# Optimization experiments

Hardware: AMD Instinct MI355X
Metric: run time of the kernel (lower is better)

## Reference

```python
import jax, jax.numpy as jnp
import numpy as np

NBINS = (128, 64, 32)
MIN_BIN_WIDTH = 1e-3
MIN_BIN_HEIGHT = 1e-3


def quadratic_spline(inputs, unnorm_widths, unnorm_heights):
    """Piecewise-quadratic CDF spline (nflows-style). inputs: (N,) in [0,1],
    unnorm_widths: (N, nb), unnorm_heights: (N, nb+1). Returns (outputs, logabsdet)."""
    num_bins = unnorm_widths.shape[-1]
    widths = jax.nn.softmax(unnorm_widths, axis=-1)
    widths = MIN_BIN_WIDTH + (1.0 - MIN_BIN_WIDTH * num_bins) * widths
    hexp = jnp.exp(unnorm_heights)
    # normalize piecewise-linear pdf to integrate to 1
    area = jnp.sum(0.5 * (hexp[:, :-1] + hexp[:, 1:]) * widths, axis=-1, keepdims=True)
    heights = hexp / area
    heights = MIN_BIN_HEIGHT + (1.0 - MIN_BIN_HEIGHT) * heights
    bin_cdf = jnp.cumsum(0.5 * (heights[:, :-1] + heights[:, 1:]) * widths, axis=-1)
    bin_left_cdf = jnp.pad(bin_cdf.at[:, -1].set(1.0), ((0, 0), (1, 0)))
    bin_loc = jnp.cumsum(widths, axis=-1)
    bin_locations = jnp.pad(bin_loc.at[:, -1].set(1.0), ((0, 0), (1, 0)))
    bin_idx = jnp.clip(jnp.sum((inputs[:, None] >= bin_locations).astype(jnp.int32), axis=-1) - 1,
                       0, num_bins - 1)[:, None]
    take = lambda t, i: jnp.take_along_axis(t, i, axis=-1)[:, 0]
    loc = take(bin_locations, bin_idx)
    w = take(widths, bin_idx)
    cdf = take(bin_left_cdf, bin_idx)
    hl = take(heights, bin_idx)
    hr = take(heights, bin_idx + 1)
    alpha = (inputs - loc) / w
    outputs = jnp.clip(0.5 * (hr - hl) * w * alpha * alpha + hl * w * alpha + cdf, 0.0, 1.0)
    logabsdet = jnp.log(alpha * (hr - hl) + hl)
    return outputs, logabsdet


def _forward(coordinates, clustering, delta_height_weight, delta_baseline_weight,
             unnormalized_heights, unnormalized_widths, baseline_bias,
             genes_oi, local_gene_ix, local_cellxgene_ix, localcellxgene_ix):
    n_total_genes = delta_baseline_weight.shape[0]
    # decoder
    dhw = delta_height_weight[genes_oi]                            # (G, L, K)
    mixture_delta = jnp.einsum('cl,glk->cgk', clustering, dhw)     # (C, G, K)
    baseline_delta = clustering @ delta_baseline_weight.T          # (C, n_total)
    baseline = jax.nn.softmax(jnp.log(baseline_bias)[None, :] + baseline_delta, axis=-1)
    baseline_cuts = baseline.reshape(-1)[localcellxgene_ix]        # (N,)
    delta = mixture_delta.reshape(-1, mixture_delta.shape[-1])[local_cellxgene_ix]  # (N, K)
    gene_global = genes_oi[local_gene_ix]                          # (N,)
    # quadratic spline stack log_prob (base = Uniform[0,1])
    x = coordinates
    logabsdet = jnp.zeros_like(coordinates)
    ho = 0
    wo = 0
    for n in NBINS:
        uh = unnormalized_heights[:, ho:ho + n][gene_global] + delta[:, ho:ho + n]
        uw = unnormalized_widths[:, wo:wo + n - 1][gene_global]
        x, lad = quadratic_spline(x, uw, uh)
        logabsdet = logabsdet + lad
        ho += n
        wo += n - 1
    likelihood_position = logabsdet
    likelihood_region = jnp.log(baseline_cuts) + jnp.log(jnp.asarray(n_total_genes, jnp.float32))
    elbo = -(likelihood_position + likelihood_region).sum()
    # KL regularization (scales = exp(log 1.0) = 1)
    half_log_2pi = float(0.5 * np.log(2.0 * np.pi))
    mixture_kl = -0.5 * dhw * dhw - half_log_2pi
    baseline_kl = -0.5 * jnp.square(delta_baseline_weight[genes_oi]) - half_log_2pi
    return elbo - mixture_kl.sum() - baseline_kl.sum()


def setup_inputs() -> dict:
    key = jax.random.key(0)
    ks = jax.random.split(key, 10)
    N, C, G, NT, L = 500_000, 1000, 500, 10_000, 16
    K = sum(NBINS)                # 224 heights / delta components
    W = sum(n - 1 for n in NBINS)  # 221 widths
    coordinates = jax.random.uniform(ks[0], (N,), jnp.float32, 1e-4, 1.0 - 1e-4)
    cluster_id = jax.random.randint(ks[1], (C,), 0, L)
    clustering = jax.nn.one_hot(cluster_id, L, dtype=jnp.float32)
    genes_oi = jnp.sort(jax.random.permutation(ks[2], NT)[:G]).astype(jnp.int32)
    cell_ix = jax.random.randint(ks[3], (N,), 0, C)
    local_gene_ix = jax.random.randint(ks[4], (N,), 0, G).astype(jnp.int32)
    local_cellxgene_ix = (cell_ix * G + local_gene_ix).astype(jnp.int32)
    localcellxgene_ix = (cell_ix * NT + genes_oi[local_gene_ix]).astype(jnp.int32)
    delta_height_weight = jax.random.normal(ks[5], (NT, L, K), jnp.float32) * 0.05
    delta_baseline_weight = jax.random.uniform(ks[6], (NT, L), jnp.float32, -0.25, 0.25)
    unnormalized_heights = jax.random.normal(ks[7], (NT, K), jnp.float32) * 0.1
    unnormalized_widths = jax.random.normal(ks[8], (NT, W), jnp.float32) * 0.1
    baseline_bias = jax.random.uniform(ks[9], (NT,), jnp.float32, 1e-5, 1.0)
    return {
        'coordinates': coordinates, 'clustering': clustering,
        'delta_height_weight': delta_height_weight,
        'delta_baseline_weight': delta_baseline_weight,
        'unnormalized_heights': unnormalized_heights,
        'unnormalized_widths': unnormalized_widths,
        'baseline_bias': baseline_bias,
        'genes_oi': genes_oi, 'local_gene_ix': local_gene_ix,
        'local_cellxgene_ix': local_cellxgene_ix,
        'localcellxgene_ix': localcellxgene_ix,
    }


def reference(coordinates, clustering, delta_height_weight, delta_baseline_weight,
              unnormalized_heights, unnormalized_widths, baseline_bias,
              genes_oi, local_gene_ix, local_cellxgene_ix, localcellxgene_ix):
    return _forward(coordinates, clustering, delta_height_weight, delta_baseline_weight,
                    unnormalized_heights, unnormalized_widths, baseline_bias,
                    genes_oi, local_gene_ix, local_cellxgene_ix, localcellxgene_ix)
```

## Files before the change

### kernel.cpp

```cpp
#include <hip/hip_runtime.h>
#include <math.h>


#define CAP 192
static constexpr float  F_MBW = 1e-3f;
static constexpr float  F_MBH = 1e-3f;
static constexpr double D_HL2PI = 0.918938533204672741780329736406;


__global__ void __launch_bounds__(256)
kA(const float* __restrict__ clustering, int* __restrict__ cid,
   double* __restrict__ dpart, int* __restrict__ cnt, int C, int L, int P) {
  int bid = blockIdx.x, tid = threadIdx.x;
  if (bid < 4) {
    int c = bid * 256 + tid;
    if (c < C) {
      const float* row = clustering + (size_t)c * L;
      int best = 0; float bv = row[0];
      for (int l = 1; l < L; ++l) { float v = row[l]; if (v > bv) { bv = v; best = l; } }
      cid[c] = best;
    }
  } else {
    if (bid == 4 && tid < 128) dpart[tid] = 0.0;
    int i = (bid - 4) * 256 + tid;
    if (i < P) cnt[i] = 0;
  }
}

__global__ void __launch_bounds__(256)
kB(const float* __restrict__ coords, const int* __restrict__ lgi,
   const int* __restrict__ lcg, const int* __restrict__ cid,
   const float* __restrict__ bb, const float* __restrict__ dbw,
   int* __restrict__ cnt, float* __restrict__ xs, double* __restrict__ dpart,
   int N, int G, int L, int NT, int SCAT) {
  int bid = blockIdx.x;
  if (bid < SCAT) {
    int base = bid * 512;
    #pragma unroll
    for (int q = 0; q < 2; ++q) {
      int n = base + q * 256 + threadIdx.x;
      if (n < N) {
        int pair = lgi[n] * L + cid[lcg[n] / G];
        int pos = atomicAdd(&cnt[pair], 1);
        if (pos < CAP) xs[(size_t)pair * CAP + pos] = coords[n];
      }
    }
  } else {
    int g = (bid - SCAT) * 256 + threadIdx.x;
    float s[16];
    #pragma unroll
    for (int l = 0; l < 16; ++l) s[l] = 0.f;
    if (g < NT) {
      float b = bb[g];
      const float4* row = (const float4*)(dbw + (size_t)g * 16);
      #pragma unroll
      for (int q = 0; q < 4; ++q) {
        float4 v = row[q];
        s[4 * q + 0] = b * expf(v.x); s[4 * q + 1] = b * expf(v.y);
        s[4 * q + 2] = b * expf(v.z); s[4 * q + 3] = b * expf(v.w);
      }
    }
    __shared__ float partl[4][16];
    int lane = threadIdx.x & 63, wv = threadIdx.x >> 6;
    #pragma unroll
    for (int l = 0; l < 16; ++l) {
      float v = s[l];
      for (int off = 32; off; off >>= 1) v += __shfl_xor(v, off);
      if (lane == 0) partl[wv][l] = v;
    }
    __syncthreads();
    if (threadIdx.x < 16) {
      float t = partl[0][threadIdx.x] + partl[1][threadIdx.x]
              + partl[2][threadIdx.x] + partl[3][threadIdx.x];
      atomicAdd(&dpart[threadIdx.x * 8], (double)t);
    }
  }
}

static __device__ __forceinline__ void wscan3(float& x, float& y, float& z, int lane) {
  #pragma unroll
  for (int off = 1; off < 64; off <<= 1) {
    float a = __shfl_up(x, off, 64);
    float b = __shfl_up(y, off, 64);
    float c = __shfl_up(z, off, 64);
    if (lane >= off) { x += a; y += b; z += c; }
  }
}

__global__ void __launch_bounds__(64)
k_pair(const float* __restrict__ uh, const float* __restrict__ uw,
       const float* __restrict__ dhw, const int* __restrict__ genes_oi,
       const float* __restrict__ xs, const int* __restrict__ cnt,
       const float* __restrict__ bb, const float* __restrict__ dbw,
       const double* __restrict__ dpart,
       float* __restrict__ partA, float* __restrict__ partB,
       int L, int K, int W, int NT) {
  int p = blockIdx.x;
  int g = p / L;
  int cl = p - g * L;
  int gg = genes_oi[g];
  const float* uhg  = uh + (size_t)gg * K;
  const float* uwg  = uw + (size_t)gg * W;
  const float* drow = dhw + ((size_t)gg * L + cl) * K;
  int t = threadIdx.x;

  __shared__ float s_loc[224];
  __shared__ float s_cdf[224];
  __shared__ float s_hh[224];
  __shared__ int   grd[224];

  const float chh = 1.0f - F_MBH;
  float d2;

  {
    const float cw128 = 1.0f - F_MBW * 127.0f;
    int i0 = 2 * t, i1 = 2 * t + 1;
    float2 dv = *(const float2*)(drow + i0);
    float2 uv = *(const float2*)(uhg + i0);
    d2 = dv.x * dv.x + dv.y * dv.y;
    float h0 = expf(uv.x + dv.x), h1 = expf(uv.y + dv.y);
    float h2 = __shfl_down(h0, 1, 64);
    float ew0 = expf(uwg[i0]);
    float ew1 = (i1 < 127) ? expf(uwg[i1]) : 0.f;
    float a0 = 0.5f * (h0 + h1);
    float a1 = (i1 < 127) ? 0.5f * (h1 + h2) : 0.f;
    float b0 = a0 * ew0, b1 = a1 * ew1;
    float sew = ew0 + ew1, sa = a0 + a1, sb = b0 + b1;
    wscan3(sew, sa, sb, t);
    float wsum = __shfl(sew, 63);
    float S1   = __shfl(sa, 63);
    float S2   = __shfl(sb, 63);
    float rw = cw128 / wsum;
    float area = F_MBW * S1 + rw * S2;
    float ra = chh / area;
    float E0 = sew - (ew0 + ew1), E1 = E0 + ew0;
    float A0 = sa - (a0 + a1),    A1 = A0 + a0;
    float B0 = sb - (b0 + b1),    B1 = B0 + b0;
    float loc0 = F_MBW * (float)i0 + rw * E0;
    float loc1 = F_MBW * (float)i1 + rw * E1;
    float cdf0 = F_MBH * loc0 + ra * (F_MBW * A0 + rw * B0);
    float cdf1 = F_MBH * loc1 + ra * (F_MBW * A1 + rw * B1);
    if (i1 == 127) { loc1 = 1.0f; cdf1 = 1.0f; }
    s_loc[i0] = loc0; s_cdf[i0] = cdf0; s_hh[i0] = F_MBH + ra * h0;
    s_loc[i1] = loc1; s_cdf[i1] = cdf1; s_hh[i1] = F_MBH + ra * h1;
  }

  int ho = 128, wo = 127, tb = 128;
  #pragma unroll
  for (int lev = 1; lev < 3; ++lev) {
    const int nbp1 = (lev == 1) ? 64 : 32;
    const int nb = nbp1 - 1;
    const float cwl = 1.0f - F_MBW * (float)nb;
    float dvx = (t < nbp1) ? drow[ho + t] : 0.f;
    d2 += dvx * dvx;
    float hexp = (t < nbp1) ? expf(uhg[ho + t] + dvx) : 0.f;
    float hn = __shfl_down(hexp, 1, 64);
    float ew = (t < nb) ? expf(uwg[wo + t]) : 0.f;
    float a  = (t < nb) ? 0.5f * (hexp + hn) : 0.f;
    float b  = a * ew;
    float sew = ew, sa = a, sb = b;
    wscan3(sew, sa, sb, t);
    float wsum = __shfl(sew, 63);
    float S1   = __shfl(sa, 63);
    float S2   = __shfl(sb, 63);
    float rw = cwl / wsum;
    float area = F_MBW * S1 + rw * S2;
    float ra = chh / area;
    float E = sew - ew, A = sa - a, B = sb - b;
    float loc = F_MBW * (float)t + rw * E;
    float cdf = F_MBH * loc + ra * (F_MBW * A + rw * B);
    float h = F_MBH + ra * hexp;
    if (t == nb) { loc = 1.0f; cdf = 1.0f; }
    if (t < nbp1) { s_loc[tb + t] = loc; s_cdf[tb + t] = cdf; s_hh[tb + t] = h; }
    ho += nbp1; wo += nb; tb += nbp1;
  }
  __syncthreads();

  {
    #pragma unroll
    for (int q = 0; q < 2; ++q) {
      int j = 2 * t + q;
      float target = (float)j * (1.0f / 128.0f);
      int lo = 0, hi = 128;
      #pragma unroll
      for (int it = 0; it < 7; ++it) {
        int mid = (lo + hi) >> 1;
        if (s_loc[mid] <= target) lo = mid; else hi = mid;
      }
      grd[j] = (lo > 126) ? 126 : lo;
    }
    {
      float target = (float)t * (1.0f / 64.0f);
      int lo = 0, hi = 64;
      #pragma unroll
      for (int it = 0; it < 6; ++it) {
        int mid = (lo + hi) >> 1;
        if (s_loc[128 + mid] <= target) lo = mid; else hi = mid;
      }
      grd[128 + t] = (lo > 62) ? 62 : lo;
    }
    if (t < 32) {
      float target = (float)t * (1.0f / 32.0f);
      int lo = 0, hi = 32;
      #pragma unroll
      for (int it = 0; it < 5; ++it) {
        int mid = (lo + hi) >> 1;
        if (s_loc[192 + mid] <= target) lo = mid; else hi = mid;
      }
      grd[192 + t] = (lo > 30) ? 30 : lo;
    }
  }
  __syncthreads();

  int m = cnt[p]; if (m > CAP) m = CAP;
  float lad_sum = 0.f;
  for (int i = t; i < m; i += 64) {
    float x = xs[(size_t)p * CAP + i];
    float lad = 0.f;
    int b2 = 0;
    #pragma unroll
    for (int lev = 0; lev < 3; ++lev) {
      const int nbp1 = (lev == 0) ? 128 : (lev == 1) ? 64 : 32;
      int j = (int)(x * (float)nbp1);
      j = (j > nbp1 - 1) ? (nbp1 - 1) : j;
      int idx = grd[b2 + j];
      while (idx > 0 && s_loc[b2 + idx] > x) --idx;
      while (idx < nbp1 - 2 && s_loc[b2 + idx + 1] <= x) ++idx;
      float la = s_loc[b2 + idx];
      float w  = s_loc[b2 + idx + 1] - la;
      float cd = s_cdf[b2 + idx];
      float hl = s_hh[b2 + idx];
      float hr = s_hh[b2 + idx + 1];
      float alpha = (x - la) / w;
      float dh = hr - hl;
      float outv = (0.5f * dh * alpha + hl) * (w * alpha) + cd;
      x = fminf(fmaxf(outv, 0.f), 1.f);
      lad += logf(alpha * dh + hl);
      b2 += nbp1;
    }
    lad_sum += lad;
  }
  #pragma unroll
  for (int off = 32; off; off >>= 1) {
    lad_sum += __shfl_xor(lad_sum, off);
    d2      += __shfl_xor(d2, off);
  }
  if (t == 0) {
    float dv = dbw[(size_t)gg * L + cl];
    float rc = logf(bb[gg]) + dv - logf((float)dpart[cl * 8]) + logf((float)NT);
    partA[p] = lad_sum + (float)m * rc;
    partB[p] = d2 + dv * dv;
  }
}

__global__ void __launch_bounds__(1024)
k_final(const float* __restrict__ partA, const float* __restrict__ partB,
        float* __restrict__ out, int P, long long M12) {
  int tid = threadIdx.x;
  double sa = 0.0, sb = 0.0;
  for (int i = tid; i < P; i += 1024) { sa += (double)partA[i]; sb += (double)partB[i]; }
  __shared__ double rA[1024], rB[1024];
  rA[tid] = sa; rB[tid] = sb;
  __syncthreads();
  for (int off = 512; off > 0; off >>= 1) {
    if (tid < off) { rA[tid] += rA[tid + off]; rB[tid] += rB[tid + off]; }
    __syncthreads();
  }
  if (tid == 0)
    out[0] = (float)(-rA[0] + 0.5 * rB[0] + (double)M12 * D_HL2PI);
}

extern "C" void kernel_launch(void* const* d_in, const int* in_sizes, int n_in,
                              void* d_out, int out_size, void* d_ws, size_t ws_size,
                              hipStream_t stream) {
  const float* coords     = (const float*)d_in[0];
  const float* clustering = (const float*)d_in[1];
  const float* dhw        = (const float*)d_in[2];
  const float* dbw        = (const float*)d_in[3];
  const float* uh         = (const float*)d_in[4];
  const float* uw         = (const float*)d_in[5];
  const float* bb         = (const float*)d_in[6];
  const int*   genes_oi   = (const int*)d_in[7];
  const int*   lgi        = (const int*)d_in[8];
  const int*   lcg        = (const int*)d_in[9];

  int N  = in_sizes[0];
  int NT = in_sizes[6];
  int L  = in_sizes[3] / NT;
  int C  = in_sizes[1] / L;
  int K  = in_sizes[4] / NT;
  int W  = in_sizes[5] / NT;
  int G  = in_sizes[7];
  int P  = G * L;

  char* ws = (char*)d_ws;
  double* dpart = (double*)ws;
  int*    cid   = (int*)(ws + 4096);
  int*    cnt   = (int*)(ws + 8192);
  float*  partA = (float*)(ws + 40960);
  float*  partB = (float*)(ws + 73728);
  float*  xs    = (float*)(ws + 131072);

  int SCAT = (N + 511) / 512;
  int LSEB = (NT + 255) / 256;

  hipLaunchKernelGGL(kA, dim3(4 + (P + 255) / 256), dim3(256), 0, stream,
                     clustering, cid, dpart, cnt, C, L, P);
  hipLaunchKernelGGL(kB, dim3(SCAT + LSEB), dim3(256), 0, stream,
                     coords, lgi, lcg, cid, bb, dbw, cnt, xs, dpart,
                     N, G, L, NT, SCAT);
  hipLaunchKernelGGL(k_pair, dim3(P), dim3(64), 0, stream,
                     uh, uw, dhw, genes_oi, xs, cnt, bb, dbw, dpart,
                     partA, partB, L, K, W, NT);
  hipLaunchKernelGGL(k_final, dim3(1), dim3(1024), 0, stream,
                     partA, partB, (float*)d_out, P,
                     (long long)G * L * K + (long long)G * L);
}
```

Before: 55.41 us.

## Pack four pairs per block, build bin grid by scatter, use fast exp/log

Each k_pair block now runs four (gene, cluster) pairs, one per wavefront, with per-wave shared tables, and launches P/4 blocks of 256 threads. The per-grid-cell binary search plus its extra barrier is replaced by each bin writing its own range of grid cells directly. expf/logf become __expf/__logf intrinsics, and the level-1/2 total-sum shuffle now reads lane nb-1. The four-pair packing assumes P is divisible by 4, and the fast intrinsics may change numerical accuracy.

```diff
diff --git a/kernel.cpp b/kernel.cpp
--- a/kernel.cpp
+++ b/kernel.cpp
@@ -40,9 +40,10 @@
     for (int q = 0; q < 2; ++q) {
       int n = base + q * 256 + threadIdx.x;
       if (n < N) {
+        float x = coords[n];
         int pair = lgi[n] * L + cid[lcg[n] / G];
         int pos = atomicAdd(&cnt[pair], 1);
-        if (pos < CAP) xs[(size_t)pair * CAP + pos] = coords[n];
+        if (pos < CAP) xs[(size_t)pair * CAP + pos] = x;
       }
     }
   } else {
@@ -87,7 +88,7 @@
   }
 }
 
-__global__ void __launch_bounds__(64)
+__global__ void __launch_bounds__(256)
 k_pair(const float* __restrict__ uh, const float* __restrict__ uw,
        const float* __restrict__ dhw, const int* __restrict__ genes_oi,
        const float* __restrict__ xs, const int* __restrict__ cnt,
@@ -95,19 +96,20 @@
        const double* __restrict__ dpart,
        float* __restrict__ partA, float* __restrict__ partB,
        int L, int K, int W, int NT) {
-  int p = blockIdx.x;
+  int wv = threadIdx.x >> 6;
+  int t  = threadIdx.x & 63;
+  int p = blockIdx.x * 4 + wv;
   int g = p / L;
   int cl = p - g * L;
   int gg = genes_oi[g];
   const float* uhg  = uh + (size_t)gg * K;
   const float* uwg  = uw + (size_t)gg * W;
   const float* drow = dhw + ((size_t)gg * L + cl) * K;
-  int t = threadIdx.x;
-
-  __shared__ float s_loc[224];
-  __shared__ float s_cdf[224];
-  __shared__ float s_hh[224];
-  __shared__ int   grd[224];
+
+  __shared__ float s_loc[4][224];
+  __shared__ float s_cdf[4][224];
+  __shared__ float s_hh[4][224];
+  __shared__ int   grd[4][224];
 
   const float chh = 1.0f - F_MBH;
   float d2;
@@ -118,10 +120,10 @@
     float2 dv = *(const float2*)(drow + i0);
     float2 uv = *(const float2*)(uhg + i0);
     d2 = dv.x * dv.x + dv.y * dv.y;
-    float h0 = expf(uv.x + dv.x), h1 = expf(uv.y + dv.y);
+    float h0 = __expf(uv.x + dv.x), h1 = __expf(uv.y + dv.y);
     float h2 = __shfl_down(h0, 1, 64);
-    float ew0 = expf(uwg[i0]);
-    float ew1 = (i1 < 127) ? expf(uwg[i1]) : 0.f;
+    float ew0 = __expf(uwg[i0]);
+    float ew1 = (i1 < 127) ? __expf(uwg[i1]) : 0.f;
     float a0 = 0.5f * (h0 + h1);
     float a1 = (i1 < 127) ? 0.5f * (h1 + h2) : 0.f;
     float b0 = a0 * ew0, b1 = a1 * ew1;
@@ -141,8 +143,15 @@
     float cdf0 = F_MBH * loc0 + ra * (F_MBW * A0 + rw * B0);
     float cdf1 = F_MBH * loc1 + ra * (F_MBW * A1 + rw * B1);
     if (i1 == 127) { loc1 = 1.0f; cdf1 = 1.0f; }
-    s_loc[i0] = loc0; s_cdf[i0] = cdf0; s_hh[i0] = F_MBH + ra * h0;
-    s_loc[i1] = loc1; s_cdf[i1] = cdf1; s_hh[i1] = F_MBH + ra * h1;
+    s_loc[wv][i0] = loc0; s_cdf[wv][i0] = cdf0; s_hh[wv][i0] = F_MBH + ra * h0;
+    s_loc[wv][i1] = loc1; s_cdf[wv][i1] = cdf1; s_hh[wv][i1] = F_MBH + ra * h1;
+    float locN = __shfl_down(loc0, 1, 64);
+    int j0 = (int)ceilf(loc0 * 128.f);
+    int j1 = (int)ceilf(loc1 * 128.f);
+    int j2 = (int)ceilf(locN * 128.f);
+    j1 = (j1 > 128) ? 128 : j1; j2 = (j2 > 128) ? 128 : j2;
+    for (int j = j0; j < j1; ++j) grd[wv][j] = i0;
+    if (i1 < 127) for (int j = j1; j < j2; ++j) grd[wv][j] = i1;
   }
 
   int ho = 128, wo = 127, tb = 128;
@@ -151,18 +160,19 @@
     const int nbp1 = (lev == 1) ? 64 : 32;
     const int nb = nbp1 - 1;
     const float cwl = 1.0f - F_MBW * (float)nb;
+    const float fn = (float)nbp1;
     float dvx = (t < nbp1) ? drow[ho + t] : 0.f;
     d2 += dvx * dvx;
-    float hexp = (t < nbp1) ? expf(uhg[ho + t] + dvx) : 0.f;
+    float hexp = (t < nbp1) ? __expf(uhg[ho + t] + dvx) : 0.f;
     float hn = __shfl_down(hexp, 1, 64);
-    float ew = (t < nb) ? expf(uwg[wo + t]) : 0.f;
+    float ew = (t < nb) ? __expf(uwg[wo + t]) : 0.f;
     float a  = (t < nb) ? 0.5f * (hexp + hn) : 0.f;
     float b  = a * ew;
     float sew = ew, sa = a, sb = b;
     wscan3(sew, sa, sb, t);
-    float wsum = __shfl(sew, 63);
-    float S1   = __shfl(sa, 63);
-    float S2   = __shfl(sb, 63);
+    float wsum = __shfl(sew, nb - 1);
+    float S1   = __shfl(sa, nb - 1);
+    float S2   = __shfl(sb, nb - 1);
     float rw = cwl / wsum;
     float area = F_MBW * S1 + rw * S2;
     float ra = chh / area;
@@ -171,47 +181,22 @@
     float cdf = F_MBH * loc + ra * (F_MBW * A + rw * B);
     float h = F_MBH + ra * hexp;
     if (t == nb) { loc = 1.0f; cdf = 1.0f; }
-    if (t < nbp1) { s_loc[tb + t] = loc; s_cdf[tb + t] = cdf; s_hh[tb + t] = h; }
+    if (t < nbp1) { s_loc[wv][tb + t] = loc; s_cdf[wv][tb + t] = cdf; s_hh[wv][tb + t] = h; }
+    float locN = __shfl_down(loc, 1, 64);
+    if (t < nb) {
+      int j0 = (int)ceilf(loc * fn);
+      int j1 = (int)ceilf(locN * fn);
+      j1 = (j1 > nbp1) ? nbp1 : j1;
+      for (int j = j0; j < j1; ++j) grd[wv][tb + j] = t;
+    }
     ho += nbp1; wo += nb; tb += nbp1;
   }
   __syncthreads();
 
-  {
-    #pragma unroll
-    for (int q = 0; q < 2; ++q) {
-      int j = 2 * t + q;
-      float target = (float)j * (1.0f / 128.0f);
-      int lo = 0, hi = 128;
-      #pragma unroll
-      for (int it = 0; it < 7; ++it) {
-        int mid = (lo + hi) >> 1;
-        if (s_loc[mid] <= target) lo = mid; else hi = mid;
-      }
-      grd[j] = (lo > 126) ? 126 : lo;
-    }
-    {
-      float target = (float)t * (1.0f / 64.0f);
-      int lo = 0, hi = 64;
-      #pragma unroll
-      for (int it = 0; it < 6; ++it) {
-        int mid = (lo + hi) >> 1;
-        if (s_loc[128 + mid] <= target) lo = mid; else hi = mid;
-      }
-      grd[128 + t] = (lo > 62) ? 62 : lo;
-    }
-    if (t < 32) {
-      float target = (float)t * (1.0f / 32.0f);
-      int lo = 0, hi = 32;
-      #pragma unroll
-      for (int it = 0; it < 5; ++it) {
-        int mid = (lo + hi) >> 1;
-        if (s_loc[192 + mid] <= target) lo = mid; else hi = mid;
-      }
-      grd[192 + t] = (lo > 30) ? 30 : lo;
-    }
-  }
-  __syncthreads();
-
+  const float* sl = s_loc[wv];
+  const float* sc = s_cdf[wv];
+  const float* sh = s_hh[wv];
+  const int*   sg = grd[wv];
   int m = cnt[p]; if (m > CAP) m = CAP;
   float lad_sum = 0.f;
   for (int i = t; i < m; i += 64) {
@@ -223,19 +208,19 @@
       const int nbp1 = (lev == 0) ? 128 : (lev == 1) ? 64 : 32;
       int j = (int)(x * (float)nbp1);
       j = (j > nbp1 - 1) ? (nbp1 - 1) : j;
-      int idx = grd[b2 + j];
-      while (idx > 0 && s_loc[b2 + idx] > x) --idx;
-      while (idx < nbp1 - 2 && s_loc[b2 + idx + 1] <= x) ++idx;
-      float la = s_loc[b2 + idx];
-      float w  = s_loc[b2 + idx + 1] - la;
-      float cd = s_cdf[b2 + idx];
-      float hl = s_hh[b2 + idx];
-      float hr = s_hh[b2 + idx + 1];
+      int idx = sg[b2 + j];
+      while (idx > 0 && sl[b2 + idx] > x) --idx;
+      while (idx < nbp1 - 2 && sl[b2 + idx + 1] <= x) ++idx;
+      float la = sl[b2 + idx];
+      float w  = sl[b2 + idx + 1] - la;
+      float cd = sc[b2 + idx];
+      float hl = sh[b2 + idx];
+      float hr = sh[b2 + idx + 1];
       float alpha = (x - la) / w;
       float dh = hr - hl;
       float outv = (0.5f * dh * alpha + hl) * (w * alpha) + cd;
       x = fminf(fmaxf(outv, 0.f), 1.f);
-      lad += logf(alpha * dh + hl);
+      lad += __logf(alpha * dh + hl);
       b2 += nbp1;
     }
     lad_sum += lad;
@@ -247,7 +232,7 @@
   }
   if (t == 0) {
     float dv = dbw[(size_t)gg * L + cl];
-    float rc = logf(bb[gg]) + dv - logf((float)dpart[cl * 8]) + logf((float)NT);
+    float rc = __logf(bb[gg]) + dv - __logf((float)dpart[cl * 8]) + __logf((float)NT);
     partA[p] = lad_sum + (float)m * rc;
     partB[p] = d2 + dv * dv;
   }
@@ -309,7 +294,7 @@
   hipLaunchKernelGGL(kB, dim3(SCAT + LSEB), dim3(256), 0, stream,
                      coords, lgi, lcg, cid, bb, dbw, cnt, xs, dpart,
                      N, G, L, NT, SCAT);
-  hipLaunchKernelGGL(k_pair, dim3(P), dim3(64), 0, stream,
+  hipLaunchKernelGGL(k_pair, dim3(P / 4), dim3(256), 0, stream,
                      uh, uw, dhw, genes_oi, xs, cnt, bb, dbw, dpart,
                      partA, partB, L, K, W, NT);
   hipLaunchKernelGGL(k_final, dim3(1), dim3(1024), 0, stream,
```

New measurement: 55.44 us. Within noise of the previous version (+0.0%).
